# Optimization experiments

Measured on AMD Instinct MI355X. Metric: run time of the kernel, lower is better.

## Reference

```python
import jax, jax.numpy as jnp
import numpy as np

DIM = 1024
N_HEADS = 16
D_HEAD = DIM // N_HEADS


def setup_inputs() -> dict:
    key = jax.random.key(0)
    ks = jax.random.split(key, 7)
    s = DIM ** -0.5
    return {
        "x": jax.random.normal(ks[0], (4, 2048, DIM), dtype=jnp.float32),
        "Wq": jax.random.normal(ks[1], (DIM, DIM), dtype=jnp.float32) * s,
        "bq": jax.random.normal(ks[2], (DIM,), dtype=jnp.float32) * 0.02,
        "Wk": jax.random.normal(ks[3], (DIM, DIM), dtype=jnp.float32) * s,
        "bk": jax.random.normal(ks[4], (DIM,), dtype=jnp.float32) * 0.02,
        "Wv": jax.random.normal(ks[5], (DIM, DIM), dtype=jnp.float32) * s,
        "bv": jax.random.normal(ks[6], (DIM,), dtype=jnp.float32) * 0.02,
    }


def reference(x, Wq, bq, Wk, bk, Wv, bv):
    B, N, D = x.shape
    H, Dh = N_HEADS, D_HEAD

    def split_heads(t):
        # b n (h d) -> b h n d
        return t.reshape(B, N, H, Dh).transpose(0, 2, 1, 3)

    q = split_heads(x @ Wq + bq)
    k = split_heads(x @ Wk + bk)
    v = split_heads(x @ Wv + bv)

    scale = Dh ** -0.5
    logit = jnp.einsum("bhnd,bhmd->bhnm", q, k) * scale  # [B,H,N,N]
    attn = jax.nn.softmax(logit, axis=-1)
    out = jnp.einsum("bhnm,bhmd->bhnd", attn, v)
    # b h n d -> b n (h d)
    return out.transpose(0, 2, 1, 3).reshape(B, N, D)
```

## Files before the change

### kernel.cpp

```cpp
#include <hip/hip_runtime.h>
#include <hip/hip_bf16.h>
#include <stdint.h>

#define BB 4
#define SEQ 2048
#define DIM 1024
#define NH 16
#define DH 64
#define MM (BB*SEQ)

typedef unsigned short u16;
typedef __attribute__((ext_vector_type(8))) __bf16 bf16x8;
typedef __attribute__((ext_vector_type(4))) float floatx4;
typedef __attribute__((ext_vector_type(4))) unsigned short u16x4;
typedef __attribute__((ext_vector_type(4))) short short4v;

#define QSCALE 0.18033688011112042f

__device__ __forceinline__ u16 f2bf(float f) {
    union { float f; unsigned u; } v; v.f = f;
    unsigned u = v.u;
    u += 0x7FFF + ((u >> 16) & 1);
    return (u16)(u >> 16);
}

__device__ __forceinline__ bf16x8 ldb8(const u16* p) {
    return *(const bf16x8*)(const void*)p;
}

__device__ __forceinline__ void async_copy16(const u16* g, u16* l) {
    __builtin_amdgcn_global_load_lds(
        (const __attribute__((address_space(1))) unsigned int*)g,
        (__attribute__((address_space(3))) unsigned int*)l, 16, 0, 0);
}

__device__ __forceinline__ floatx4 mfma16(short4v a, short4v b, floatx4 c) {
    return __builtin_amdgcn_mfma_f32_16x16x16bf16_1k(a, b, c, 0, 0, 0);
}

__global__ __launch_bounds__(256)
void prep(const float* __restrict__ x, u16* __restrict__ xb,
          const float* __restrict__ Wq, const float* __restrict__ Wk,
          const float* __restrict__ Wv, u16* __restrict__ Wt) {
    const int bx = blockIdx.x;
    const int tid = threadIdx.x;
    if (bx < 8192) {
        const size_t i = ((size_t)bx * 256 + tid) * 4;
        float4 f = *(const float4*)(x + i);
        u16x4 o = { f2bf(f.x), f2bf(f.y), f2bf(f.z), f2bf(f.w) };
        *(u16x4*)(xb + i) = o;
        return;
    }
    const int idx = bx - 8192;
    const int t = idx >> 8;
    const int r2 = idx & 255;
    const int k0 = (r2 >> 4) * 64, n0 = (r2 & 15) * 64;
    const float* W = (t == 0) ? Wq : (t == 1) ? Wk : Wv;
    u16* D = Wt + (size_t)t * DIM * DIM;
    __shared__ u16 T[64][65];
    #pragma unroll
    for (int p = 0; p < 4; p++) {
        const int r = p * 16 + (tid >> 4), c = (tid & 15) * 4;
        float4 f = *(const float4*)(W + (size_t)(k0 + r) * DIM + n0 + c);
        T[c + 0][r] = f2bf(f.x); T[c + 1][r] = f2bf(f.y);
        T[c + 2][r] = f2bf(f.z); T[c + 3][r] = f2bf(f.w);
    }
    __syncthreads();
    #pragma unroll
    for (int p = 0; p < 4; p++) {
        const int rn = p * 16 + (tid >> 4), ck = (tid & 15) * 4;
        u16x4 v = { T[rn][ck], T[rn][ck + 1], T[rn][ck + 2], T[rn][ck + 3] };
        *(u16x4*)(D + (size_t)(n0 + rn) * DIM + k0 + ck) = v;
    }
}

__global__ __launch_bounds__(256, 3)
void qkv_gemm3(const u16* __restrict__ xb, const u16* __restrict__ Wt,
               const float* __restrict__ bq, const float* __restrict__ bk,
               const float* __restrict__ bv, u16* __restrict__ ws) {
    __shared__ u16 As[2][4096];
    __shared__ u16 Bs[2][4096];

    const int m0 = blockIdx.x * 128;
    const int t  = blockIdx.y >> 3;
    const int c0 = (blockIdx.y & 7) * 128;
    const u16* Wtb = Wt + (size_t)t * DIM * DIM;
    const float* bias = (t == 0) ? bq : (t == 1) ? bk : bv;
    const float osc = (t == 0) ? QSCALE : 1.0f;
    u16* dst = ws + (size_t)t * ((size_t)MM * DIM);

    const int tid  = threadIdx.x;
    const int lane = tid & 63;
    const int w    = tid >> 6;
    const int wr = w >> 1, wc = w & 1;
    const int g = lane >> 4, ln = lane & 15;

    floatx4 acc[4][4];
    #pragma unroll
    for (int i = 0; i < 4; i++)
        #pragma unroll
        for (int j = 0; j < 4; j++) acc[i][j] = (floatx4){0.f,0.f,0.f,0.f};

    const int srow = w*16 + (lane >> 2);
    const int gseg = (lane & 3) ^ ((lane >> 3) & 3);
    const u16* gA = xb  + (size_t)(m0 + srow) * DIM + gseg*8;
    const u16* gB = Wtb + (size_t)(c0 + srow) * DIM + gseg*8;

    async_copy16(gA,                   &As[0][w*512]);
    async_copy16(gA + (size_t)64*DIM,  &As[0][2048 + w*512]);
    async_copy16(gB,                   &Bs[0][w*512]);
    async_copy16(gB + (size_t)64*DIM,  &Bs[0][2048 + w*512]);
    __syncthreads();

    const int xu = (ln >> 1) & 3;

    for (int it = 0; it < 32; it++) {
        const int cur = it & 1;
        if (it < 31) {
            const int nxt = cur ^ 1;
            const int kk = (it + 1) * 32;
            async_copy16(gA + kk,                  &As[nxt][w*512]);
            async_copy16(gA + kk + (size_t)64*DIM, &As[nxt][2048 + w*512]);
            async_copy16(gB + kk,                  &Bs[nxt][w*512]);
            async_copy16(gB + kk + (size_t)64*DIM, &Bs[nxt][2048 + w*512]);
        }

        bf16x8 a[4], b[4];
        #pragma unroll
        for (int fr = 0; fr < 4; fr++)
            a[fr] = ldb8(&As[cur][(wr*64 + fr*16 + ln)*32 + (g ^ xu)*8]);
        #pragma unroll
        for (int fc = 0; fc < 4; fc++)
            b[fc] = ldb8(&Bs[cur][(wc*64 + fc*16 + ln)*32 + (g ^ xu)*8]);

        if (t < 2) {
            #pragma unroll
            for (int fr = 0; fr < 4; fr++)
                #pragma unroll
                for (int fc = 0; fc < 4; fc++)
                    acc[fr][fc] = __builtin_amdgcn_mfma_f32_16x16x32_bf16(
                        b[fc], a[fr], acc[fr][fc], 0, 0, 0);
        } else {
            #pragma unroll
            for (int fr = 0; fr < 4; fr++)
                #pragma unroll
                for (int fc = 0; fc < 4; fc++)
                    acc[fr][fc] = __builtin_amdgcn_mfma_f32_16x16x32_bf16(
                        a[fr], b[fc], acc[fr][fc], 0, 0, 0);
        }
        __syncthreads();
    }

    if (t < 2) {
        #pragma unroll
        for (int fc = 0; fc < 4; fc++) {
            const int cc = c0 + wc*64 + fc*16 + g*4;
            const float4 b4 = *(const float4*)&bias[cc];
            const int h = cc >> 6, d = cc & 63;
            #pragma unroll
            for (int fr = 0; fr < 4; fr++) {
                const int tok = m0 + wr*64 + fr*16 + ln;
                const int bidx = tok >> 11, nn = tok & 2047;
                u16x4 v = { f2bf((acc[fr][fc][0] + b4.x) * osc),
                            f2bf((acc[fr][fc][1] + b4.y) * osc),
                            f2bf((acc[fr][fc][2] + b4.z) * osc),
                            f2bf((acc[fr][fc][3] + b4.w) * osc) };
                *(u16x4*)&dst[((size_t)(bidx*NH + h)*SEQ + nn)*DH + d] = v;
            }
        }
    } else {
        #pragma unroll
        for (int fc = 0; fc < 4; fc++) {
            const int cc = c0 + wc*64 + fc*16 + ln;
            const float bias_v = bias[cc];
            const int h = cc >> 6, d = cc & 63;
            #pragma unroll
            for (int fr = 0; fr < 4; fr++) {
                const int mrow = m0 + wr*64 + fr*16 + g*4;
                const int bidx = mrow >> 11, nn = mrow & 2047;
                u16x4 v = { f2bf(acc[fr][fc][0] + bias_v), f2bf(acc[fr][fc][1] + bias_v),
                            f2bf(acc[fr][fc][2] + bias_v), f2bf(acc[fr][fc][3] + bias_v) };
                *(u16x4*)&dst[((size_t)(bidx*NH + h)*DH + d)*SEQ + nn] = v;
            }
        }
    }
}

#define LDA 40
__global__ __launch_bounds__(256)
void qkv_gemm(const float* __restrict__ x,
              const float* __restrict__ Wq, const float* __restrict__ bq,
              const float* __restrict__ Wk, const float* __restrict__ bk,
              const float* __restrict__ Wv, const float* __restrict__ bv,
              u16* __restrict__ ws) {
    __shared__ u16 As[128 * LDA];
    __shared__ u16 Bs[128 * LDA];
    const int m0 = blockIdx.x * 128;
    const int t  = blockIdx.y >> 3;
    const int c0 = (blockIdx.y & 7) * 128;
    const float* W    = (t == 0) ? Wq : (t == 1) ? Wk : Wv;
    const float* bias = (t == 0) ? bq : (t == 1) ? bk : bv;
    const float osc = (t == 0) ? QSCALE : 1.0f;
    u16* dst = ws + (size_t)t * ((size_t)MM * DIM);
    const int tid  = threadIdx.x;
    const int lane = tid & 63;
    const int wave = tid >> 6;
    const int wr = wave >> 1, wc = wave & 1;
    const int g = lane >> 4, ln = lane & 15;
    floatx4 acc[4][4];
    #pragma unroll
    for (int i = 0; i < 4; i++)
        #pragma unroll
        for (int j = 0; j < 4; j++) acc[i][j] = (floatx4){0.f,0.f,0.f,0.f};
    const int ar  = tid >> 1;
    const int ak  = (tid & 1) * 16;
    const int bkr = tid & 31;
    const int bc  = (tid >> 5) * 16;
    for (int kk = 0; kk < DIM; kk += 32) {
        {
            const float4* s4 = (const float4*)(x + (size_t)(m0 + ar) * DIM + kk + ak);
            float4 f0 = s4[0], f1 = s4[1], f2 = s4[2], f3 = s4[3];
            unsigned pk[8];
            pk[0] = f2bf(f0.x) | ((unsigned)f2bf(f0.y) << 16);
            pk[1] = f2bf(f0.z) | ((unsigned)f2bf(f0.w) << 16);
            pk[2] = f2bf(f1.x) | ((unsigned)f2bf(f1.y) << 16);
            pk[3] = f2bf(f1.z) | ((unsigned)f2bf(f1.w) << 16);
            pk[4] = f2bf(f2.x) | ((unsigned)f2bf(f2.y) << 16);
            pk[5] = f2bf(f2.z) | ((unsigned)f2bf(f2.w) << 16);
            pk[6] = f2bf(f3.x) | ((unsigned)f2bf(f3.y) << 16);
            pk[7] = f2bf(f3.z) | ((unsigned)f2bf(f3.w) << 16);
            uint4* d = (uint4*)&As[ar * LDA + ak];
            d[0] = make_uint4(pk[0], pk[1], pk[2], pk[3]);
            d[1] = make_uint4(pk[4], pk[5], pk[6], pk[7]);
        }
        {
            const float4* s4 = (const float4*)(W + (size_t)(kk + bkr) * DIM + c0 + bc);
            float4 f0 = s4[0], f1 = s4[1], f2 = s4[2], f3 = s4[3];
            float fv[16] = {f0.x,f0.y,f0.z,f0.w, f1.x,f1.y,f1.z,f1.w,
                            f2.x,f2.y,f2.z,f2.w, f3.x,f3.y,f3.z,f3.w};
            #pragma unroll
            for (int j = 0; j < 16; j++)
                Bs[(bc + j) * LDA + bkr] = f2bf(fv[j]);
        }
        __syncthreads();
        bf16x8 a[4], b[4];
        #pragma unroll
        for (int fr = 0; fr < 4; fr++)
            a[fr] = ldb8(&As[(wr*64 + fr*16 + ln) * LDA + g*8]);
        #pragma unroll
        for (int fc = 0; fc < 4; fc++)
            b[fc] = ldb8(&Bs[(wc*64 + fc*16 + ln) * LDA + g*8]);
        #pragma unroll
        for (int fr = 0; fr < 4; fr++)
            #pragma unroll
            for (int fc = 0; fc < 4; fc++)
                acc[fr][fc] = __builtin_amdgcn_mfma_f32_16x16x32_bf16(
                    a[fr], b[fc], acc[fr][fc], 0, 0, 0);
        __syncthreads();
    }
    #pragma unroll
    for (int fc = 0; fc < 4; fc++) {
        const int cc = c0 + wc*64 + fc*16 + ln;
        const float bias_v = bias[cc];
        const int h = cc >> 6, d = cc & 63;
        #pragma unroll
        for (int fr = 0; fr < 4; fr++) {
            #pragma unroll
            for (int rr = 0; rr < 4; rr++) {
                const int mrow = m0 + wr*64 + fr*16 + g*4 + rr;
                const int bidx = mrow >> 11, nn = mrow & 2047;
                const float val = (acc[fr][fc][rr] + bias_v) * osc;
                size_t idx;
                if (t < 2) idx = ((size_t)(bidx*NH + h)*SEQ + nn)*DH + d;
                else       idx = ((size_t)(bidx*NH + h)*DH + d)*SEQ + nn;
                dst[idx] = f2bf(val);
            }
        }
    }
}

__global__ __launch_bounds__(256, 4)
void attn6(const u16* __restrict__ ws, float* __restrict__ out) {
    const int qt = blockIdx.x;
    const int h  = blockIdx.y;
    const int b  = blockIdx.z;
    const int bh = b*NH + h;

    const u16* Qw = ws;
    const u16* Kw = ws + (size_t)MM * DIM;
    const u16* Vt = ws + 2 * (size_t)MM * DIM;

    __shared__ u16 Kbuf[2][4096];
    __shared__ u16 Vbuf[2][4096];

    const int tid  = threadIdx.x;
    const int lane = tid & 63;
    const int w    = tid >> 6;
    const int g = lane >> 4, ln = lane & 15;
    const int q0 = qt*128 + w*32;

    const int srow = w*8 + (lane >> 3);
    const int sseg = (lane & 7) ^ ((lane >> 3) & 7);
    const u16* kg = Kw + ((size_t)bh*SEQ + srow)*DH + sseg*8;
    const u16* vg = Vt + ((size_t)bh*DH + srow)*SEQ + sseg*8;

    const int fs0 = ((0*4 + g) ^ (ln & 7)) * 8;
    const int fs1 = ((1*4 + g) ^ (ln & 7)) * 8;
    const int vxor = ln & 7;
    const int gh = g >> 1;
    const int vh = (g & 1) * 4;

    bf16x8 aq[2][2];
    #pragma unroll
    for (int rb = 0; rb < 2; rb++) {
        const u16* qp = Qw + ((size_t)bh*SEQ + q0 + rb*16 + ln)*DH + g*8;
        aq[rb][0] = ldb8(qp);
        aq[rb][1] = ldb8(qp + 32);
    }

    floatx4 acc[2][4];
    #pragma unroll
    for (int rb = 0; rb < 2; rb++)
        #pragma unroll
        for (int i = 0; i < 4; i++) acc[rb][i] = (floatx4){0.f,0.f,0.f,0.f};
    float lrun[2] = {0.f, 0.f};

    async_copy16(kg,                  &Kbuf[0][w*512]);
    async_copy16(kg + (size_t)32*DH,  &Kbuf[0][2048 + w*512]);
    async_copy16(vg,                  &Vbuf[0][w*512]);
    async_copy16(vg + (size_t)32*SEQ, &Vbuf[0][2048 + w*512]);
    __syncthreads();

    for (int kt = 0; kt < 32; kt++) {
        const int cur = kt & 1;
        if (kt < 31) {
            const int nxt = cur ^ 1;
            const size_t ko = (size_t)(kt + 1) * 64 * DH;
            const size_t vo = (size_t)(kt + 1) * 64;
            async_copy16(kg + ko,                  &Kbuf[nxt][w*512]);
            async_copy16(kg + ko + (size_t)32*DH,  &Kbuf[nxt][2048 + w*512]);
            async_copy16(vg + vo,                  &Vbuf[nxt][w*512]);
            async_copy16(vg + vo + (size_t)32*SEQ, &Vbuf[nxt][2048 + w*512]);
        }

        const u16* Kc = &Kbuf[cur][0];
        const u16* Vc = &Vbuf[cur][0];

        #pragma unroll
        for (int fn = 0; fn < 4; fn++) {
            bf16x8 k0 = ldb8(&Kc[(fn*16 + ln)*64 + fs0]);
            bf16x8 k1 = ldb8(&Kc[(fn*16 + ln)*64 + fs1]);
            short4v bp[2];
            #pragma unroll
            for (int rb = 0; rb < 2; rb++) {
                floatx4 z = (floatx4){0.f,0.f,0.f,0.f};
                z = __builtin_amdgcn_mfma_f32_16x16x32_bf16(k0, aq[rb][0], z, 0, 0, 0);
                z = __builtin_amdgcn_mfma_f32_16x16x32_bf16(k1, aq[rb][1], z, 0, 0, 0);
                float p0 = __builtin_amdgcn_exp2f(z[0]);
                float p1 = __builtin_amdgcn_exp2f(z[1]);
                float p2 = __builtin_amdgcn_exp2f(z[2]);
                float p3 = __builtin_amdgcn_exp2f(z[3]);
                lrun[rb] += (p0 + p1) + (p2 + p3);
                union { __hip_bfloat162 h2[2]; short4v s4; } pu;
                pu.h2[0] = __float22bfloat162_rn(make_float2(p0, p1));
                pu.h2[1] = __float22bfloat162_rn(make_float2(p2, p3));
                bp[rb] = pu.s4;
            }
            const int vu = ((fn*2 + gh) ^ vxor) * 8 + vh;
            #pragma unroll
            for (int fd = 0; fd < 4; fd++) {
                short4v av = *(const short4v*)(const void*)&Vc[(fd*16 + ln)*64 + vu];
                acc[0][fd] = mfma16(av, bp[0], acc[0][fd]);
                acc[1][fd] = mfma16(av, bp[1], acc[1][fd]);
            }
        }
        __syncthreads();
    }

    #pragma unroll
    for (int rb = 0; rb < 2; rb++) {
        float v = lrun[rb];
        v += __shfl_xor(v, 16, 64);
        v += __shfl_xor(v, 32, 64);
        const float inv = 1.0f / v;
        const int n = q0 + rb*16 + ln;
        #pragma unroll
        for (int fd = 0; fd < 4; fd++) {
            floatx4 vv = acc[rb][fd];
            float4 o = { vv[0]*inv, vv[1]*inv, vv[2]*inv, vv[3]*inv };
            *(float4*)&out[((size_t)b*SEQ + n)*DIM + h*DH + fd*16 + g*4] = o;
        }
    }
}

extern "C" void kernel_launch(void* const* d_in, const int* in_sizes, int n_in,
                              void* d_out, int out_size, void* d_ws, size_t ws_size,
                              hipStream_t stream) {
    const float* x  = (const float*)d_in[0];
    const float* Wq = (const float*)d_in[1];
    const float* bq = (const float*)d_in[2];
    const float* Wk = (const float*)d_in[3];
    const float* bk = (const float*)d_in[4];
    const float* Wv = (const float*)d_in[5];
    const float* bv = (const float*)d_in[6];
    u16* ws = (u16*)d_ws;
    float* out = (float*)d_out;

    const size_t need = (size_t)4 * MM * DIM * 2 + (size_t)3 * DIM * DIM * 2;
    if (ws_size >= need) {
        u16* xb = ws + (size_t)3 * MM * DIM;
        u16* Wt = ws + (size_t)4 * MM * DIM;
        prep<<<dim3(8192 + 768), 256, 0, stream>>>(x, xb, Wq, Wk, Wv, Wt);
        qkv_gemm3<<<dim3(MM/128, 24), 256, 0, stream>>>(xb, Wt, bq, bk, bv, ws);
    } else {
        qkv_gemm<<<dim3(MM/128, 24), 256, 0, stream>>>(x, Wq, bq, Wk, bk, Wv, bv, ws);
    }
    attn6<<<dim3(SEQ/128, NH, BB), 256, 0, stream>>>(ws, out);
}
```

Measured before the change: 269.6 us.

## Split attention block across 8 waves with 16 query rows each

The attention kernel now launches 512 threads per block (8 waves) instead of 256, and each wave handles 16 query rows instead of 32. The K/V tile load is spread over 8 waves, one 16-byte copy each per tile. The aim is more waves in flight and lower per-thread register use to hide latency. In exchange, each K/V fragment read from LDS now feeds only one MFMA per wave instead of two, which lowers reuse and raises LDS traffic per unit of compute.

```diff
diff --git a/kernel.cpp b/kernel.cpp
--- a/kernel.cpp
+++ b/kernel.cpp
@@ -279,8 +279,8 @@
     }
 }
 
-__global__ __launch_bounds__(256, 4)
-void attn6(const u16* __restrict__ ws, float* __restrict__ out) {
+__global__ __launch_bounds__(512, 8)
+void attn7(const u16* __restrict__ ws, float* __restrict__ out) {
     const int qt = blockIdx.x;
     const int h  = blockIdx.y;
     const int b  = blockIdx.z;
@@ -297,7 +297,7 @@
     const int lane = tid & 63;
     const int w    = tid >> 6;
     const int g = lane >> 4, ln = lane & 15;
-    const int q0 = qt*128 + w*32;
+    const int q0 = qt*128 + w*16;
 
     const int srow = w*8 + (lane >> 3);
     const int sseg = (lane & 7) ^ ((lane >> 3) & 7);
@@ -310,25 +310,20 @@
     const int gh = g >> 1;
     const int vh = (g & 1) * 4;
 
-    bf16x8 aq[2][2];
-    #pragma unroll
-    for (int rb = 0; rb < 2; rb++) {
-        const u16* qp = Qw + ((size_t)bh*SEQ + q0 + rb*16 + ln)*DH + g*8;
-        aq[rb][0] = ldb8(qp);
-        aq[rb][1] = ldb8(qp + 32);
-    }
-
-    floatx4 acc[2][4];
-    #pragma unroll
-    for (int rb = 0; rb < 2; rb++)
-        #pragma unroll
-        for (int i = 0; i < 4; i++) acc[rb][i] = (floatx4){0.f,0.f,0.f,0.f};
-    float lrun[2] = {0.f, 0.f};
-
-    async_copy16(kg,                  &Kbuf[0][w*512]);
-    async_copy16(kg + (size_t)32*DH,  &Kbuf[0][2048 + w*512]);
-    async_copy16(vg,                  &Vbuf[0][w*512]);
-    async_copy16(vg + (size_t)32*SEQ, &Vbuf[0][2048 + w*512]);
+    bf16x8 aq0, aq1;
+    {
+        const u16* qp = Qw + ((size_t)bh*SEQ + q0 + ln)*DH + g*8;
+        aq0 = ldb8(qp);
+        aq1 = ldb8(qp + 32);
+    }
+
+    floatx4 acc[4];
+    #pragma unroll
+    for (int i = 0; i < 4; i++) acc[i] = (floatx4){0.f,0.f,0.f,0.f};
+    float lrun = 0.f;
+
+    async_copy16(kg, &Kbuf[0][w*512]);
+    async_copy16(vg, &Vbuf[0][w*512]);
     __syncthreads();
 
     for (int kt = 0; kt < 32; kt++) {
@@ -337,10 +332,8 @@
             const int nxt = cur ^ 1;
             const size_t ko = (size_t)(kt + 1) * 64 * DH;
             const size_t vo = (size_t)(kt + 1) * 64;
-            async_copy16(kg + ko,                  &Kbuf[nxt][w*512]);
-            async_copy16(kg + ko + (size_t)32*DH,  &Kbuf[nxt][2048 + w*512]);
-            async_copy16(vg + vo,                  &Vbuf[nxt][w*512]);
-            async_copy16(vg + vo + (size_t)32*SEQ, &Vbuf[nxt][2048 + w*512]);
+            async_copy16(kg + ko, &Kbuf[nxt][w*512]);
+            async_copy16(vg + vo, &Vbuf[nxt][w*512]);
         }
 
         const u16* Kc = &Kbuf[cur][0];
@@ -350,43 +343,38 @@
         for (int fn = 0; fn < 4; fn++) {
             bf16x8 k0 = ldb8(&Kc[(fn*16 + ln)*64 + fs0]);
             bf16x8 k1 = ldb8(&Kc[(fn*16 + ln)*64 + fs1]);
-            short4v bp[2];
-            #pragma unroll
-            for (int rb = 0; rb < 2; rb++) {
-                floatx4 z = (floatx4){0.f,0.f,0.f,0.f};
-                z = __builtin_amdgcn_mfma_f32_16x16x32_bf16(k0, aq[rb][0], z, 0, 0, 0);
-                z = __builtin_amdgcn_mfma_f32_16x16x32_bf16(k1, aq[rb][1], z, 0, 0, 0);
-                float p0 = __builtin_amdgcn_exp2f(z[0]);
-                float p1 = __builtin_amdgcn_exp2f(z[1]);
-                float p2 = __builtin_amdgcn_exp2f(z[2]);
-                float p3 = __builtin_amdgcn_exp2f(z[3]);
-                lrun[rb] += (p0 + p1) + (p2 + p3);
-                union { __hip_bfloat162 h2[2]; short4v s4; } pu;
-                pu.h2[0] = __float22bfloat162_rn(make_float2(p0, p1));
-                pu.h2[1] = __float22bfloat162_rn(make_float2(p2, p3));
-                bp[rb] = pu.s4;
-            }
+            floatx4 z = (floatx4){0.f,0.f,0.f,0.f};
+            z = __builtin_amdgcn_mfma_f32_16x16x32_bf16(k0, aq0, z, 0, 0, 0);
+            z = __builtin_amdgcn_mfma_f32_16x16x32_bf16(k1, aq1, z, 0, 0, 0);
+            float p0 = __builtin_amdgcn_exp2f(z[0]);
+            float p1 = __builtin_amdgcn_exp2f(z[1]);
+            float p2 = __builtin_amdgcn_exp2f(z[2]);
+            float p3 = __builtin_amdgcn_exp2f(z[3]);
+            lrun += (p0 + p1) + (p2 + p3);
+            union { __hip_bfloat162 h2[2]; short4v s4; } pu;
+            pu.h2[0] = __float22bfloat162_rn(make_float2(p0, p1));
+            pu.h2[1] = __float22bfloat162_rn(make_float2(p2, p3));
+            const short4v bp = pu.s4;
+
             const int vu = ((fn*2 + gh) ^ vxor) * 8 + vh;
             #pragma unroll
             for (int fd = 0; fd < 4; fd++) {
                 short4v av = *(const short4v*)(const void*)&Vc[(fd*16 + ln)*64 + vu];
-                acc[0][fd] = mfma16(av, bp[0], acc[0][fd]);
-                acc[1][fd] = mfma16(av, bp[1], acc[1][fd]);
+                acc[fd] = mfma16(av, bp, acc[fd]);
             }
         }
         __syncthreads();
     }
 
-    #pragma unroll
-    for (int rb = 0; rb < 2; rb++) {
-        float v = lrun[rb];
+    {
+        float v = lrun;
         v += __shfl_xor(v, 16, 64);
         v += __shfl_xor(v, 32, 64);
         const float inv = 1.0f / v;
-        const int n = q0 + rb*16 + ln;
+        const int n = q0 + ln;
         #pragma unroll
         for (int fd = 0; fd < 4; fd++) {
-            floatx4 vv = acc[rb][fd];
+            floatx4 vv = acc[fd];
             float4 o = { vv[0]*inv, vv[1]*inv, vv[2]*inv, vv[3]*inv };
             *(float4*)&out[((size_t)b*SEQ + n)*DIM + h*DH + fd*16 + g*4] = o;
         }
@@ -415,5 +403,5 @@
     } else {
         qkv_gemm<<<dim3(MM/128, 24), 256, 0, stream>>>(x, Wq, bq, Wk, bk, Wv, bv, ws);
     }
-    attn6<<<dim3(SEQ/128, NH, BB), 256, 0, stream>>>(ws, out);
-}
+    attn7<<<dim3(SEQ/128, NH, BB), 512, 0, stream>>>(ws, out);
+}
```

Measured after the change: 277.2 us. 2.8% more time.
